# Kernel optimization log

Measured on AMD Instinct MI355X. Metric: run time of the kernel, lower is better.

Reference implementation:

```python
import jax, jax.numpy as jnp
import numpy as np
import math

B, T, C, H = 4, 1024, 1024, 16
D = C // H
EPS = 1e-5


def layer_norm(x, w, b):
    mu = jnp.mean(x, axis=-1, keepdims=True)
    var = jnp.mean(jnp.square(x - mu), axis=-1, keepdims=True)
    return (x - mu) * jax.lax.rsqrt(var + EPS) * w + b


def setup_inputs() -> dict:
    key = jax.random.key(0)
    ks = jax.random.split(key, 8)
    s = 0.02
    return {
        "x": jax.random.normal(ks[0], (B, T, C), jnp.float32),
        "attention_mask": jnp.ones((B, T), jnp.float32),
        "ln1_w": jnp.ones((C,), jnp.float32),
        "ln1_b": jnp.zeros((C,), jnp.float32),
        "w_attn": jax.random.normal(ks[1], (C, 3 * C), jnp.float32) * s,
        "b_attn": jnp.zeros((3 * C,), jnp.float32),
        "w_proj": jax.random.normal(ks[2], (C, C), jnp.float32) * s,
        "b_proj": jnp.zeros((C,), jnp.float32),
        "threshold": jnp.float32(0.0005),  # (layer_idx+1)/n_layer * final_token_threshold
        "ln2_w": jnp.ones((C,), jnp.float32),
        "ln2_b": jnp.zeros((C,), jnp.float32),
        "w_fc": jax.random.normal(ks[3], (C, 4 * C), jnp.float32) * s,
        "b_fc": jnp.zeros((4 * C,), jnp.float32),
        "w_fc2": jax.random.normal(ks[4], (4 * C, C), jnp.float32) * s,
        "b_fc2": jnp.zeros((C,), jnp.float32),
    }


def reference(x, attention_mask, ln1_w, ln1_b, w_attn, b_attn, w_proj, b_proj,
              threshold, ln2_w, ln2_b, w_fc, b_fc, w_fc2, b_fc2):
    # ---- attention (eval mode, dropout=0; hard masking_mode) ----
    h = layer_norm(x, ln1_w, ln1_b)
    qkv = h @ w_attn + b_attn                      # (B,T,3C)
    q, k, v = jnp.split(qkv, 3, axis=-1)
    q = q.reshape(B, T, H, D).transpose(0, 2, 1, 3)  # (B,H,T,D)
    k = k.reshape(B, T, H, D).transpose(0, 2, 1, 3)
    v = v.reshape(B, T, H, D).transpose(0, 2, 1, 3)

    scale = 1.0 / math.sqrt(D)
    logits = jnp.einsum("bhqd,bhkd->bhqk", q, k) * scale  # (B,H,T,T)
    causal = jnp.tril(jnp.ones((T, T), bool))
    neg_inf = jnp.float32(-jnp.inf)
    logits = jnp.where(causal[None, None], logits, neg_inf)
    # key-side validity mask (applied in original's manual pass; mask is all-ones
    # here so flash-path y == softmax(causal logits) @ v as well)
    logits = jnp.where(attention_mask[:, None, None, :] == 0, neg_inf, logits)
    att = jax.nn.softmax(logits, axis=-1)

    y = jnp.einsum("bhqk,bhkd->bhqd", att, v)      # (B,H,T,D)
    importance = att.mean(axis=1).mean(axis=1)     # (B,T): mean over heads, then queries

    y = y.transpose(0, 2, 1, 3).reshape(B, T, C)
    x = x + (y @ w_proj + b_proj)

    # ---- hard pruning mask ----
    pruning_mask = (importance >= threshold).astype(x.dtype)
    combined_mask = attention_mask * pruning_mask
    x = x * combined_mask[:, :, None]

    # ---- MLP ----
    h2 = layer_norm(x, ln2_w, ln2_b)
    f = jax.nn.gelu(h2 @ w_fc + b_fc, approximate=False)
    x = x + (f @ w_fc2 + b_fc2)

    pruning_loss = jnp.float32(0.0)  # hard mode -> always 0
    return (x, combined_mask, pruning_loss)
```

## Files before the change

kernel.cpp:

```cpp
#include <hip/hip_runtime.h>
#include <cstdint>
#include <cstring>

typedef unsigned short u16;
typedef short bf16x8 __attribute__((ext_vector_type(8)));
typedef float f32x4 __attribute__((ext_vector_type(4)));

#define MFMA16(a,b,c) __builtin_amdgcn_mfma_f32_16x16x32_bf16(a,b,c,0,0,0)


__device__ __forceinline__ u16 f2bf(float f) {
  union { float f; uint32_t u; } un; un.f = f;
  uint32_t u = un.u;
  u += 0x7FFFu + ((u >> 16) & 1u);
  return (u16)(u >> 16);
}

__device__ __forceinline__ float bf2f(u16 h) {
  union { uint32_t u; float f; } un; un.u = ((uint32_t)h) << 16;
  return un.f;
}

__device__ __forceinline__ float gelu_fast(float v) {
  float u = 0.7978845608028654f * (v + 0.044715f * v * v * v);
  float e = __expf(2.f * u);
  float th = 1.f - __fdividef(2.f, e + 1.f);
  return 0.5f * v * (1.f + th);
}

__device__ __forceinline__ void gl_lds16(const void* g, void* l) {
  __builtin_amdgcn_global_load_lds(
      (__attribute__((address_space(1))) void*)(const_cast<void*>(g)),
      (__attribute__((address_space(3))) void*)l, 16, 0, 0);
}


__global__ __launch_bounds__(256) void transpose_all(
    const float* __restrict__ wa, const float* __restrict__ wp,
    const float* __restrict__ wf, const float* __restrict__ wf2,
    u16* __restrict__ wat, u16* __restrict__ wpt,
    u16* __restrict__ wft, u16* __restrict__ wf2t)
{
  __shared__ float tile[32][33];
  int id = blockIdx.x;
  const float* W; u16* Wt; int K, N, bx, by;
  if (id < 3072)      { W = wa;  Wt = wat;  K = 1024; N = 3072; bx = id % 96;  by = id / 96; }
  else if (id < 4096) { id -= 3072; W = wp;  Wt = wpt;  K = 1024; N = 1024; bx = id % 32; by = id / 32; }
  else if (id < 8192) { id -= 4096; W = wf;  Wt = wft;  K = 1024; N = 4096; bx = id % 128; by = id / 128; }
  else                { id -= 8192; W = wf2; Wt = wf2t; K = 4096; N = 1024; bx = id % 32; by = id / 32; }
  int kt = by * 32, nt = bx * 32;
  int tx = threadIdx.x, ty = threadIdx.y;
#pragma unroll
  for (int i = 0; i < 4; ++i)
    tile[ty + i * 8][tx] = W[(size_t)(kt + ty + i * 8) * N + nt + tx];
  __syncthreads();
#pragma unroll
  for (int i = 0; i < 4; ++i)
    Wt[(size_t)(nt + ty + i * 8) * K + kt + tx] = f2bf(tile[tx][ty + i * 8]);
}


__global__ __launch_bounds__(256) void ln_bf16(
    const float* __restrict__ x, const float* __restrict__ wt,
    const float* __restrict__ bs, u16* __restrict__ out)
{
  int row = blockIdx.x;
  int tid = threadIdx.x, lane = tid & 63, w = tid >> 6;
  const float* xr = x + (size_t)row * 1024;
  float4 v = *(const float4*)(xr + tid * 4);
  float s = v.x + v.y + v.z + v.w;
  float sq = v.x * v.x + v.y * v.y + v.z * v.z + v.w * v.w;
#pragma unroll
  for (int o = 1; o < 64; o <<= 1) { s += __shfl_xor(s, o); sq += __shfl_xor(sq, o); }
  __shared__ float ls[4], lq[4];
  if (lane == 0) { ls[w] = s; lq[w] = sq; }
  __syncthreads();
  s = ls[0] + ls[1] + ls[2] + ls[3];
  sq = lq[0] + lq[1] + lq[2] + lq[3];
  float mu = s * (1.f / 1024.f);
  float var = sq * (1.f / 1024.f) - mu * mu;
  float rstd = rsqrtf(var + 1e-5f);
  float4 wv = *(const float4*)(wt + tid * 4);
  float4 bv = *(const float4*)(bs + tid * 4);
  ushort4 o4;
  o4.x = f2bf((v.x - mu) * rstd * wv.x + bv.x);
  o4.y = f2bf((v.y - mu) * rstd * wv.y + bv.y);
  o4.z = f2bf((v.z - mu) * rstd * wv.z + bv.z);
  o4.w = f2bf((v.w - mu) * rstd * wv.w + bv.w);
  *(ushort4*)(out + (size_t)row * 1024 + tid * 4) = o4;
}


__device__ __forceinline__ void gemm_mainloop_db(
    const u16* __restrict__ Abase, const u16* __restrict__ Bbase,
    int lda, int ldb, int nIter, f32x4 acc[4][4])
{
  __shared__ __align__(16) u16 lA[2][128 * 32];
  __shared__ __align__(16) u16 lB[2][128 * 32];

  const int tid = threadIdx.x;
  const int lane = tid & 63;
  const int w = tid >> 6;
  const int wr = (w >> 1) * 64;
  const int wc = (w & 1) * 64;
  const int laneM = lane & 15;
  const int laneK = (lane >> 4) * 8;

#pragma unroll
  for (int i = 0; i < 4; ++i)
#pragma unroll
    for (int j = 0; j < 4; ++j)
      acc[i][j] = f32x4{0.f, 0.f, 0.f, 0.f};

  const int off0 = w * 1024 + lane * 16;
  const int off1 = off0 + 4096;
  const int rA0 = off0 >> 6, cb0 = off0 & 63;
  const int rA1 = off1 >> 6, cb1 = off1 & 63;

  const size_t sA = (size_t)lda * 2;
  const size_t sB = (size_t)ldb * 2;
  const char* pA0 = (const char*)Abase + (size_t)rA0 * sA + cb0;
  const char* pA1 = (const char*)Abase + (size_t)rA1 * sA + cb1;
  const char* pB0 = (const char*)Bbase + (size_t)rA0 * sB + cb0;
  const char* pB1 = (const char*)Bbase + (size_t)rA1 * sB + cb1;
  char* dA0 = (char*)&lA[0][0] + off0;
  char* dA1 = (char*)&lA[0][0] + off1;
  char* dB0 = (char*)&lB[0][0] + off0;
  char* dB1 = (char*)&lB[0][0] + off1;

  gl_lds16(pA0, dA0); gl_lds16(pA1, dA1);
  gl_lds16(pB0, dB0); gl_lds16(pB1, dB1);
  pA0 += 64; pA1 += 64; pB0 += 64; pB1 += 64;
  __syncthreads();

  for (int it = 0; it < nIter; ++it) {
    const int cur = it & 1;
    const int nb = cur ^ 1;
    if (it + 1 < nIter) {
      gl_lds16(pA0, dA0 + nb * 8192);
      gl_lds16(pA1, dA1 + nb * 8192);
      gl_lds16(pB0, dB0 + nb * 8192);
      gl_lds16(pB1, dB1 + nb * 8192);
      pA0 += 64; pA1 += 64; pB0 += 64; pB1 += 64;
    }
    const u16* aRd = &lA[cur][(wr + laneM) * 32 + laneK];
    const u16* bRd = &lB[cur][(wc + laneM) * 32 + laneK];
    bf16x8 af[4], bfr[4];
#pragma unroll
    for (int t = 0; t < 4; ++t) {
      af[t]  = *(const bf16x8*)(aRd + t * 16 * 32);
      bfr[t] = *(const bf16x8*)(bRd + t * 16 * 32);
    }
#pragma unroll
    for (int i = 0; i < 4; ++i)
#pragma unroll
      for (int j = 0; j < 4; ++j)
        acc[i][j] = MFMA16(af[i], bfr[j], acc[i][j]);
    if (it + 1 < nIter) __syncthreads();
  }
}


__global__ __launch_bounds__(256, 4) void gemm_qkv(
    const u16* __restrict__ A, const u16* __restrict__ Bt,
    const float* __restrict__ bias,
    u16* __restrict__ qo, u16* __restrict__ ko, u16* __restrict__ vo)
{
  f32x4 acc[4][4];
  int m0 = blockIdx.y * 128, n0 = blockIdx.x * 128;
  gemm_mainloop_db(A + (size_t)m0 * 1024, Bt + (size_t)n0 * 1024, 1024, 1024, 32, acc);
  const int lane = threadIdx.x & 63, w = threadIdx.x >> 6;
  const int wr = (w >> 1) * 64, wc = (w & 1) * 64;
  const int laneM = lane & 15, q4 = lane >> 4;
  const int which = (n0 >> 10);
#pragma unroll
  for (int ti = 0; ti < 4; ++ti) {
#pragma unroll
    for (int tj = 0; tj < 4; ++tj) {
      int n = n0 + wc + tj * 16 + laneM;
      int c = n & 1023;
      int hh = c >> 6, d = c & 63;
      float bval = bias[n];
      if (which == 2) {
        int m0r = m0 + wr + ti * 16 + q4 * 4;
        int b = m0r >> 10, t0 = m0r & 1023;
        ushort4 o4;
        o4.x = f2bf(acc[ti][tj][0] + bval);
        o4.y = f2bf(acc[ti][tj][1] + bval);
        o4.z = f2bf(acc[ti][tj][2] + bval);
        o4.w = f2bf(acc[ti][tj][3] + bval);
        *(ushort4*)&vo[((size_t)((b * 16 + hh) * 64 + d)) * 1024 + t0] = o4;
      } else {
        u16* dst = (which == 0) ? qo : ko;
#pragma unroll
        for (int r = 0; r < 4; ++r) {
          int m = m0 + wr + ti * 16 + q4 * 4 + r;
          int b = m >> 10, t = m & 1023;
          dst[((size_t)((b * 16 + hh) * 1024 + t)) * 64 + d] = f2bf(acc[ti][tj][r] + bval);
        }
      }
    }
  }
}

__global__ __launch_bounds__(256, 4) void gemm_proj(
    const u16* __restrict__ A, const u16* __restrict__ Bt,
    const float* __restrict__ bias, const float* __restrict__ xin,
    const float* __restrict__ maskv, float* __restrict__ x2)
{
  f32x4 acc[4][4];
  int m0 = blockIdx.y * 128, n0 = blockIdx.x * 128;
  gemm_mainloop_db(A + (size_t)m0 * 1024, Bt + (size_t)n0 * 1024, 1024, 1024, 32, acc);
  const int lane = threadIdx.x & 63, w = threadIdx.x >> 6;
  const int wr = (w >> 1) * 64, wc = (w & 1) * 64;
  const int laneM = lane & 15, q4 = lane >> 4;
#pragma unroll
  for (int ti = 0; ti < 4; ++ti) {
#pragma unroll
    for (int tj = 0; tj < 4; ++tj) {
      int n = n0 + wc + tj * 16 + laneM;
      float bval = bias[n];
#pragma unroll
      for (int r = 0; r < 4; ++r) {
        int m = m0 + wr + ti * 16 + q4 * 4 + r;
        float v = xin[(size_t)m * 1024 + n] + acc[ti][tj][r] + bval;
        x2[(size_t)m * 1024 + n] = v * maskv[m];
      }
    }
  }
}

__global__ __launch_bounds__(256, 4) void gemm_fc(
    const u16* __restrict__ A, const u16* __restrict__ Bt,
    const float* __restrict__ bias, u16* __restrict__ fo)
{
  f32x4 acc[4][4];
  int m0 = blockIdx.y * 128, n0 = blockIdx.x * 128;
  gemm_mainloop_db(A + (size_t)m0 * 1024, Bt + (size_t)n0 * 1024, 1024, 1024, 32, acc);
  const int lane = threadIdx.x & 63, w = threadIdx.x >> 6;
  const int wr = (w >> 1) * 64, wc = (w & 1) * 64;
  const int laneM = lane & 15, q4 = lane >> 4;
#pragma unroll
  for (int ti = 0; ti < 4; ++ti) {
#pragma unroll
    for (int tj = 0; tj < 4; ++tj) {
      int n = n0 + wc + tj * 16 + laneM;
      float bval = bias[n];
#pragma unroll
      for (int r = 0; r < 4; ++r) {
        int m = m0 + wr + ti * 16 + q4 * 4 + r;
        fo[(size_t)m * 4096 + n] = f2bf(gelu_fast(acc[ti][tj][r] + bval));
      }
    }
  }
}

__global__ __launch_bounds__(256, 4) void gemm_fc2_splitk(
    const u16* __restrict__ A, const u16* __restrict__ Bt,
    u16* __restrict__ pall)
{
  int id = blockIdx.x;
  int r = id & 7, j = id >> 3;
  int mt = r * 4 + (j >> 5);
  int rem = j & 31;
  int n0 = (rem & 7) * 128;
  int kz = rem >> 3;
  int m0 = mt * 128;
  f32x4 acc[4][4];
  gemm_mainloop_db(A + (size_t)m0 * 4096 + kz * 1024,
                   Bt + (size_t)n0 * 4096 + kz * 1024, 4096, 4096, 32, acc);
  u16* p = pall + (size_t)kz * 4096 * 1024;
  const int lane = threadIdx.x & 63, w = threadIdx.x >> 6;
  const int wr = (w >> 1) * 64, wc = (w & 1) * 64;
  const int laneM = lane & 15, q4 = lane >> 4;
#pragma unroll
  for (int ti = 0; ti < 4; ++ti) {
#pragma unroll
    for (int tj = 0; tj < 4; ++tj) {
      int n = n0 + wc + tj * 16 + laneM;
#pragma unroll
      for (int r2 = 0; r2 < 4; ++r2) {
        int m = m0 + wr + ti * 16 + q4 * 4 + r2;
        p[(size_t)m * 1024 + n] = f2bf(acc[ti][tj][r2]);
      }
    }
  }
}

__global__ __launch_bounds__(256) void fc2_finalize(
    const float* __restrict__ x2, const float* __restrict__ bias,
    const u16* __restrict__ pall, float* __restrict__ out)
{
  int i = blockIdx.x * 256 + threadIdx.x;
  int col4 = i & 255;
  float4 a = ((const float4*)x2)[i];
  float4 b = ((const float4*)bias)[col4];
  float s0 = a.x + b.x, s1 = a.y + b.y, s2 = a.z + b.z, s3 = a.w + b.w;
#pragma unroll
  for (int z = 0; z < 4; ++z) {
    ushort4 u = ((const ushort4*)(pall + (size_t)z * 4194304))[i];
    s0 += bf2f(u.x); s1 += bf2f(u.y); s2 += bf2f(u.z); s3 += bf2f(u.w);
  }
  float4 o; o.x = s0; o.y = s1; o.z = s2; o.w = s3;
  ((float4*)out)[i] = o;
}


__global__ __launch_bounds__(256) void attn_fwd(
    const u16* __restrict__ qb, const u16* __restrict__ kb, const u16* __restrict__ vtb,
    u16* __restrict__ yb, float* __restrict__ part)
{
  const int bh = blockIdx.x;
  const int qbi = 7 - blockIdx.y;
  const int b = bh >> 4, h = bh & 15;
  const int tid = threadIdx.x, lane = tid & 63, w = tid >> 6;
  const int q0 = qbi * 128;
  const int laneM = lane & 15, q4 = lane >> 4;
  const float scale = 0.125f;

  __shared__ __align__(16) u16 lK[64 * 72];
  __shared__ __align__(16) u16 lV[64 * 72];
  __shared__ __align__(16) u16 lP[4][32 * 72];

  bf16x8 qf[2][2];
#pragma unroll
  for (int qs = 0; qs < 2; ++qs) {
    const u16* qrow = qb + ((size_t)(bh * 1024 + q0 + w * 32 + qs * 16 + laneM)) * 64 + q4 * 8;
    qf[qs][0] = *(const bf16x8*)qrow;
    qf[qs][1] = *(const bf16x8*)(qrow + 32);
  }

  const int nkt = 2 * qbi + 2;
  const int srow = tid >> 3;
  const int scol = (tid & 7) * 8;
  const u16* kbase = kb + (size_t)bh * 65536;
  const u16* vbase = vtb + (size_t)bh * 65536;

  float lrow[2][4] = {{0.f,0.f,0.f,0.f},{0.f,0.f,0.f,0.f}};
  for (int kt = 0; kt < nkt; ++kt) {
#pragma unroll
    for (int p = 0; p < 2; ++p) {
      int row = srow + p * 32;
      *(uint4*)&lK[row * 72 + scol] =
          *(const uint4*)(kbase + (size_t)(kt * 64 + row) * 64 + scol);
    }
    __syncthreads();
#pragma unroll
    for (int tj = 0; tj < 4; ++tj) {
      const u16* kp = &lK[(tj * 16 + laneM) * 72 + q4 * 8];
      bf16x8 k0 = *(const bf16x8*)kp;
      bf16x8 k1 = *(const bf16x8*)(kp + 32);
      int kc = kt * 64 + tj * 16 + laneM;
#pragma unroll
      for (int qs = 0; qs < 2; ++qs) {
        f32x4 z = {0.f, 0.f, 0.f, 0.f};
        z = MFMA16(qf[qs][0], k0, z);
        z = MFMA16(qf[qs][1], k1, z);
#pragma unroll
        for (int r = 0; r < 4; ++r) {
          int qg = q0 + w * 32 + qs * 16 + q4 * 4 + r;
          lrow[qs][r] += (kc <= qg) ? __expf(z[r] * scale) : 0.f;
        }
      }
    }
    __syncthreads();
  }
  float linv[2][4];
#pragma unroll
  for (int qs = 0; qs < 2; ++qs)
#pragma unroll
    for (int r = 0; r < 4; ++r) {
      float s = lrow[qs][r];
      s += __shfl_xor(s, 1); s += __shfl_xor(s, 2);
      s += __shfl_xor(s, 4); s += __shfl_xor(s, 8);
      linv[qs][r] = 1.f / s;
    }

  f32x4 o_[2][4];
#pragma unroll
  for (int qs = 0; qs < 2; ++qs)
#pragma unroll
    for (int dt = 0; dt < 4; ++dt) o_[qs][dt] = f32x4{0.f, 0.f, 0.f, 0.f};

  for (int kt = 0; kt < nkt; ++kt) {
#pragma unroll
    for (int p = 0; p < 2; ++p) {
      int row = srow + p * 32;
      *(uint4*)&lK[row * 72 + scol] =
          *(const uint4*)(kbase + (size_t)(kt * 64 + row) * 64 + scol);
      *(uint4*)&lV[row * 72 + scol] =
          *(const uint4*)(vbase + (size_t)row * 1024 + kt * 64 + scol);
    }
    __syncthreads();
    u16* lPw = &lP[w][0];
#pragma unroll
    for (int tj = 0; tj < 4; ++tj) {
      const u16* kp = &lK[(tj * 16 + laneM) * 72 + q4 * 8];
      bf16x8 k0 = *(const bf16x8*)kp;
      bf16x8 k1 = *(const bf16x8*)(kp + 32);
      int kc = kt * 64 + tj * 16 + laneM;
      float cs = 0.f;
#pragma unroll
      for (int qs = 0; qs < 2; ++qs) {
        f32x4 z = {0.f, 0.f, 0.f, 0.f};
        z = MFMA16(qf[qs][0], k0, z);
        z = MFMA16(qf[qs][1], k1, z);
#pragma unroll
        for (int r = 0; r < 4; ++r) {
          int qg = q0 + w * 32 + qs * 16 + q4 * 4 + r;
          float pv = (kc <= qg) ? __expf(z[r] * scale) * linv[qs][r] : 0.f;
          cs += pv;
          lPw[(qs * 16 + q4 * 4 + r) * 72 + tj * 16 + laneM] = f2bf(pv);
        }
      }
      cs += __shfl_xor(cs, 16);
      cs += __shfl_xor(cs, 32);
      if (lane < 16)
        atomicAdd(&part[(size_t)bh * 1024 + kt * 64 + tj * 16 + lane], cs);
    }
#pragma unroll
    for (int ss = 0; ss < 2; ++ss) {
#pragma unroll
      for (int qs = 0; qs < 2; ++qs) {
        bf16x8 pf = *(const bf16x8*)&lP[w][(qs * 16 + laneM) * 72 + ss * 32 + q4 * 8];
#pragma unroll
        for (int dt = 0; dt < 4; ++dt) {
          bf16x8 vf = *(const bf16x8*)&lV[(dt * 16 + laneM) * 72 + ss * 32 + q4 * 8];
          o_[qs][dt] = MFMA16(pf, vf, o_[qs][dt]);
        }
      }
    }
    __syncthreads();
  }

#pragma unroll
  for (int qs = 0; qs < 2; ++qs)
#pragma unroll
    for (int dt = 0; dt < 4; ++dt)
#pragma unroll
      for (int r = 0; r < 4; ++r) {
        int qg = q0 + w * 32 + qs * 16 + q4 * 4 + r;
        yb[((size_t)(b * 1024 + qg)) * 1024 + h * 64 + dt * 16 + laneM] = f2bf(o_[qs][dt][r]);
      }
}


__global__ __launch_bounds__(256) void finalize_mask(
    const float* __restrict__ part, const float* __restrict__ amask,
    const float* __restrict__ thr, float* __restrict__ mask_ws,
    float* __restrict__ out_mask, float* __restrict__ out_loss)
{
  int i = blockIdx.x * 256 + threadIdx.x;
  if (i >= 4096) return;
  int b = i >> 10;
  int t = i & 1023;
  float s = 0.f;
#pragma unroll
  for (int hh = 0; hh < 16; ++hh) s += part[(size_t)(b * 16 + hh) * 1024 + t];
  float imp = s * (1.0f / 16384.0f);
  float mv = (imp >= thr[0]) ? amask[i] : 0.f;
  mask_ws[i] = mv;
  out_mask[i] = mv;
  if (i == 0) out_loss[0] = 0.f;
}


extern "C" void kernel_launch(void* const* d_in, const int* in_sizes, int n_in,
                              void* d_out, int out_size, void* d_ws, size_t ws_size,
                              hipStream_t stream) {
  const float* x      = (const float*)d_in[0];
  const float* amask  = (const float*)d_in[1];
  const float* ln1w   = (const float*)d_in[2];
  const float* ln1b   = (const float*)d_in[3];
  const float* w_attn = (const float*)d_in[4];
  const float* b_attn = (const float*)d_in[5];
  const float* w_proj = (const float*)d_in[6];
  const float* b_proj = (const float*)d_in[7];
  const float* thr    = (const float*)d_in[8];
  const float* ln2w   = (const float*)d_in[9];
  const float* ln2b   = (const float*)d_in[10];
  const float* w_fc   = (const float*)d_in[11];
  const float* b_fc   = (const float*)d_in[12];
  const float* w_fc2  = (const float*)d_in[13];
  const float* b_fc2  = (const float*)d_in[14];
  float* out = (float*)d_out;

  char* ws = (char*)d_ws;
  size_t off = 0;
  auto alloc = [&](size_t bytes) -> char* {
    char* p = ws + off;
    off += (bytes + 255) & ~(size_t)255;
    return p;
  };
  u16* wattnT = (u16*)alloc((size_t)3072 * 1024 * 2);
  u16* wprojT = (u16*)alloc((size_t)1024 * 1024 * 2);
  u16* wfcT   = (u16*)alloc((size_t)4096 * 1024 * 2);
  u16* wfc2T  = (u16*)alloc((size_t)1024 * 4096 * 2);
  u16* hbuf   = (u16*)alloc((size_t)4096 * 1024 * 2);
  u16* qbuf   = (u16*)alloc((size_t)64 * 1024 * 64 * 2);
  u16* kbuf   = (u16*)alloc((size_t)64 * 1024 * 64 * 2);
  u16* vtbuf  = (u16*)alloc((size_t)64 * 64 * 1024 * 2);
  u16* ybuf   = (u16*)alloc((size_t)4096 * 1024 * 2);
  float* part = (float*)alloc((size_t)64 * 1024 * 4);
  float* maskws = (float*)alloc((size_t)4096 * 4);
  float* x2   = (float*)alloc((size_t)4096 * 1024 * 4);
  u16* h2     = (u16*)alloc((size_t)4096 * 1024 * 2);
  u16* fbuf   = (u16*)alloc((size_t)4096 * 4096 * 2);

  u16* pall = qbuf;

  transpose_all<<<12288, dim3(32, 8), 0, stream>>>(
      w_attn, w_proj, w_fc, w_fc2, wattnT, wprojT, wfcT, wfc2T);

  hipMemsetAsync(part, 0, (size_t)64 * 1024 * 4, stream);

  ln_bf16<<<4096, 256, 0, stream>>>(x, ln1w, ln1b, hbuf);

  gemm_qkv<<<dim3(24, 32), 256, 0, stream>>>(hbuf, wattnT, b_attn, qbuf, kbuf, vtbuf);

  attn_fwd<<<dim3(64, 8), 256, 0, stream>>>(qbuf, kbuf, vtbuf, ybuf, part);

  finalize_mask<<<16, 256, 0, stream>>>(part, amask, thr, maskws,
                                        out + 4194304, out + 4198400);

  gemm_proj<<<dim3(8, 32), 256, 0, stream>>>(ybuf, wprojT, b_proj, x, maskws, x2);

  ln_bf16<<<4096, 256, 0, stream>>>(x2, ln2w, ln2b, h2);

  gemm_fc<<<dim3(32, 32), 256, 0, stream>>>(h2, wfcT, b_fc, fbuf);

  gemm_fc2_splitk<<<1024, 256, 0, stream>>>(fbuf, wfc2T, pall);

  fc2_finalize<<<4096, 256, 0, stream>>>(x2, b_fc2, pall, out);
}
```

Before: 353.0 us.

## Restructure attention kernel: 8 waves, double-buffered K/V, LDS column-sum accumulation

The attention kernel now runs 512 threads per block, with each wave owning 16 query rows instead of 32. K and V tiles are double-buffered in LDS, so the next tile's global load is issued before the current tile's MFMA work and stored afterwards. Per-key column sums for the importance score are gathered with shared-memory atomics and flushed to global once per block, replacing many global atomics. A 1D grid with an interleaved query-block mapping pairs long and short causal blocks to balance work across CUs. The cost is more LDS per block and more registers held for the prefetch.

Result: no change. 348.9 us (-1.2%).

```diff
diff --git a/kernel.cpp b/kernel.cpp
--- a/kernel.cpp
+++ b/kernel.cpp
@@ -306,28 +306,34 @@
 }
 
 
-__global__ __launch_bounds__(256) void attn_fwd(
+__global__ __launch_bounds__(512) void attn_fwd(
     const u16* __restrict__ qb, const u16* __restrict__ kb, const u16* __restrict__ vtb,
     u16* __restrict__ yb, float* __restrict__ part)
 {
-  const int bh = blockIdx.x;
-  const int qbi = 7 - blockIdx.y;
+  const int id = blockIdx.x;
+  const int slot = (id & 7) ^ ((id >> 8) & 1);
+  const int qbi = (slot & 1) ? (slot >> 1) : (7 - (slot >> 1));
+  const int bh = id >> 3;
   const int b = bh >> 4, h = bh & 15;
+
   const int tid = threadIdx.x, lane = tid & 63, w = tid >> 6;
   const int q0 = qbi * 128;
   const int laneM = lane & 15, q4 = lane >> 4;
   const float scale = 0.125f;
 
-  __shared__ __align__(16) u16 lK[64 * 72];
-  __shared__ __align__(16) u16 lV[64 * 72];
-  __shared__ __align__(16) u16 lP[4][32 * 72];
-
-  bf16x8 qf[2][2];
-#pragma unroll
-  for (int qs = 0; qs < 2; ++qs) {
-    const u16* qrow = qb + ((size_t)(bh * 1024 + q0 + w * 32 + qs * 16 + laneM)) * 64 + q4 * 8;
-    qf[qs][0] = *(const bf16x8*)qrow;
-    qf[qs][1] = *(const bf16x8*)(qrow + 32);
+  __shared__ __align__(16) u16 lK[2][64 * 72];
+  __shared__ __align__(16) u16 lV[2][64 * 72];
+  __shared__ __align__(16) u16 lP[8][16 * 72];
+  __shared__ float part_s[1024];
+
+  part_s[tid] = 0.f;
+  part_s[tid + 512] = 0.f;
+
+  bf16x8 qf[2];
+  {
+    const u16* qrow = qb + ((size_t)(bh * 1024 + q0 + w * 16 + laneM)) * 64 + q4 * 8;
+    qf[0] = *(const bf16x8*)qrow;
+    qf[1] = *(const bf16x8*)(qrow + 32);
   }
 
   const int nkt = 2 * qbi + 2;
@@ -336,112 +342,109 @@
   const u16* kbase = kb + (size_t)bh * 65536;
   const u16* vbase = vtb + (size_t)bh * 65536;
 
-  float lrow[2][4] = {{0.f,0.f,0.f,0.f},{0.f,0.f,0.f,0.f}};
-  for (int kt = 0; kt < nkt; ++kt) {
-#pragma unroll
-    for (int p = 0; p < 2; ++p) {
-      int row = srow + p * 32;
-      *(uint4*)&lK[row * 72 + scol] =
-          *(const uint4*)(kbase + (size_t)(kt * 64 + row) * 64 + scol);
-    }
+  float lrow[4] = {0.f, 0.f, 0.f, 0.f};
+  {
+    uint4 pk = *(const uint4*)(kbase + (size_t)srow * 64 + scol);
+    *(uint4*)&lK[0][srow * 72 + scol] = pk;
     __syncthreads();
-#pragma unroll
-    for (int tj = 0; tj < 4; ++tj) {
-      const u16* kp = &lK[(tj * 16 + laneM) * 72 + q4 * 8];
-      bf16x8 k0 = *(const bf16x8*)kp;
-      bf16x8 k1 = *(const bf16x8*)(kp + 32);
-      int kc = kt * 64 + tj * 16 + laneM;
-#pragma unroll
-      for (int qs = 0; qs < 2; ++qs) {
+    for (int kt = 0; kt < nkt; ++kt) {
+      const int cur = kt & 1;
+      if (kt + 1 < nkt)
+        pk = *(const uint4*)(kbase + (size_t)((kt + 1) * 64 + srow) * 64 + scol);
+#pragma unroll
+      for (int tj = 0; tj < 4; ++tj) {
+        const u16* kp = &lK[cur][(tj * 16 + laneM) * 72 + q4 * 8];
+        bf16x8 k0 = *(const bf16x8*)kp;
+        bf16x8 k1 = *(const bf16x8*)(kp + 32);
         f32x4 z = {0.f, 0.f, 0.f, 0.f};
-        z = MFMA16(qf[qs][0], k0, z);
-        z = MFMA16(qf[qs][1], k1, z);
+        z = MFMA16(qf[0], k0, z);
+        z = MFMA16(qf[1], k1, z);
+        int kc = kt * 64 + tj * 16 + laneM;
 #pragma unroll
         for (int r = 0; r < 4; ++r) {
-          int qg = q0 + w * 32 + qs * 16 + q4 * 4 + r;
-          lrow[qs][r] += (kc <= qg) ? __expf(z[r] * scale) : 0.f;
+          int qg = q0 + w * 16 + q4 * 4 + r;
+          lrow[r] += (kc <= qg) ? __expf(z[r] * scale) : 0.f;
         }
       }
-    }
+      if (kt + 1 < nkt) *(uint4*)&lK[cur ^ 1][srow * 72 + scol] = pk;
+      __syncthreads();
+    }
+  }
+  float linv[4];
+#pragma unroll
+  for (int r = 0; r < 4; ++r) {
+    float s = lrow[r];
+    s += __shfl_xor(s, 1); s += __shfl_xor(s, 2);
+    s += __shfl_xor(s, 4); s += __shfl_xor(s, 8);
+    linv[r] = 1.f / s;
+  }
+
+  f32x4 o_[4];
+#pragma unroll
+  for (int dt = 0; dt < 4; ++dt) o_[dt] = f32x4{0.f, 0.f, 0.f, 0.f};
+
+  {
+    uint4 pk = *(const uint4*)(kbase + (size_t)srow * 64 + scol);
+    uint4 pv = *(const uint4*)(vbase + (size_t)srow * 1024 + scol);
+    *(uint4*)&lK[0][srow * 72 + scol] = pk;
+    *(uint4*)&lV[0][srow * 72 + scol] = pv;
     __syncthreads();
-  }
-  float linv[2][4];
-#pragma unroll
-  for (int qs = 0; qs < 2; ++qs)
+    for (int kt = 0; kt < nkt; ++kt) {
+      const int cur = kt & 1;
+      if (kt + 1 < nkt) {
+        pk = *(const uint4*)(kbase + (size_t)((kt + 1) * 64 + srow) * 64 + scol);
+        pv = *(const uint4*)(vbase + (size_t)srow * 1024 + (kt + 1) * 64 + scol);
+      }
+      u16* lPw = &lP[w][0];
+#pragma unroll
+      for (int tj = 0; tj < 4; ++tj) {
+        const u16* kp = &lK[cur][(tj * 16 + laneM) * 72 + q4 * 8];
+        bf16x8 k0 = *(const bf16x8*)kp;
+        bf16x8 k1 = *(const bf16x8*)(kp + 32);
+        f32x4 z = {0.f, 0.f, 0.f, 0.f};
+        z = MFMA16(qf[0], k0, z);
+        z = MFMA16(qf[1], k1, z);
+        int kc = kt * 64 + tj * 16 + laneM;
+        float cs = 0.f;
+#pragma unroll
+        for (int r = 0; r < 4; ++r) {
+          int qg = q0 + w * 16 + q4 * 4 + r;
+          float pvf = (kc <= qg) ? __expf(z[r] * scale) * linv[r] : 0.f;
+          cs += pvf;
+          lPw[(q4 * 4 + r) * 72 + tj * 16 + laneM] = f2bf(pvf);
+        }
+        cs += __shfl_xor(cs, 16);
+        cs += __shfl_xor(cs, 32);
+        if (lane < 16) atomicAdd(&part_s[kt * 64 + tj * 16 + lane], cs);
+      }
+#pragma unroll
+      for (int ss = 0; ss < 2; ++ss) {
+        bf16x8 pf = *(const bf16x8*)&lP[w][laneM * 72 + ss * 32 + q4 * 8];
+#pragma unroll
+        for (int dt = 0; dt < 4; ++dt) {
+          bf16x8 vf = *(const bf16x8*)&lV[cur][(dt * 16 + laneM) * 72 + ss * 32 + q4 * 8];
+          o_[dt] = MFMA16(pf, vf, o_[dt]);
+        }
+      }
+      if (kt + 1 < nkt) {
+        *(uint4*)&lK[cur ^ 1][srow * 72 + scol] = pk;
+        *(uint4*)&lV[cur ^ 1][srow * 72 + scol] = pv;
+      }
+      __syncthreads();
+    }
+  }
+
+  const int kmax = nkt * 64;
+  for (int i = tid; i < kmax; i += 512)
+    atomicAdd(&part[(size_t)bh * 1024 + i], part_s[i]);
+
+#pragma unroll
+  for (int dt = 0; dt < 4; ++dt)
 #pragma unroll
     for (int r = 0; r < 4; ++r) {
-      float s = lrow[qs][r];
-      s += __shfl_xor(s, 1); s += __shfl_xor(s, 2);
-      s += __shfl_xor(s, 4); s += __shfl_xor(s, 8);
-      linv[qs][r] = 1.f / s;
-    }
-
-  f32x4 o_[2][4];
-#pragma unroll
-  for (int qs = 0; qs < 2; ++qs)
-#pragma unroll
-    for (int dt = 0; dt < 4; ++dt) o_[qs][dt] = f32x4{0.f, 0.f, 0.f, 0.f};
-
-  for (int kt = 0; kt < nkt; ++kt) {
-#pragma unroll
-    for (int p = 0; p < 2; ++p) {
-      int row = srow + p * 32;
-      *(uint4*)&lK[row * 72 + scol] =
-          *(const uint4*)(kbase + (size_t)(kt * 64 + row) * 64 + scol);
-      *(uint4*)&lV[row * 72 + scol] =
-          *(const uint4*)(vbase + (size_t)row * 1024 + kt * 64 + scol);
-    }
-    __syncthreads();
-    u16* lPw = &lP[w][0];
-#pragma unroll
-    for (int tj = 0; tj < 4; ++tj) {
-      const u16* kp = &lK[(tj * 16 + laneM) * 72 + q4 * 8];
-      bf16x8 k0 = *(const bf16x8*)kp;
-      bf16x8 k1 = *(const bf16x8*)(kp + 32);
-      int kc = kt * 64 + tj * 16 + laneM;
-      float cs = 0.f;
-#pragma unroll
-      for (int qs = 0; qs < 2; ++qs) {
-        f32x4 z = {0.f, 0.f, 0.f, 0.f};
-        z = MFMA16(qf[qs][0], k0, z);
-        z = MFMA16(qf[qs][1], k1, z);
-#pragma unroll
-        for (int r = 0; r < 4; ++r) {
-          int qg = q0 + w * 32 + qs * 16 + q4 * 4 + r;
-          float pv = (kc <= qg) ? __expf(z[r] * scale) * linv[qs][r] : 0.f;
-          cs += pv;
-          lPw[(qs * 16 + q4 * 4 + r) * 72 + tj * 16 + laneM] = f2bf(pv);
-        }
-      }
-      cs += __shfl_xor(cs, 16);
-      cs += __shfl_xor(cs, 32);
-      if (lane < 16)
-        atomicAdd(&part[(size_t)bh * 1024 + kt * 64 + tj * 16 + lane], cs);
-    }
-#pragma unroll
-    for (int ss = 0; ss < 2; ++ss) {
-#pragma unroll
-      for (int qs = 0; qs < 2; ++qs) {
-        bf16x8 pf = *(const bf16x8*)&lP[w][(qs * 16 + laneM) * 72 + ss * 32 + q4 * 8];
-#pragma unroll
-        for (int dt = 0; dt < 4; ++dt) {
-          bf16x8 vf = *(const bf16x8*)&lV[(dt * 16 + laneM) * 72 + ss * 32 + q4 * 8];
-          o_[qs][dt] = MFMA16(pf, vf, o_[qs][dt]);
-        }
-      }
-    }
-    __syncthreads();
-  }
-
-#pragma unroll
-  for (int qs = 0; qs < 2; ++qs)
-#pragma unroll
-    for (int dt = 0; dt < 4; ++dt)
-#pragma unroll
-      for (int r = 0; r < 4; ++r) {
-        int qg = q0 + w * 32 + qs * 16 + q4 * 4 + r;
-        yb[((size_t)(b * 1024 + qg)) * 1024 + h * 64 + dt * 16 + laneM] = f2bf(o_[qs][dt][r]);
-      }
+      int qg = q0 + w * 16 + q4 * 4 + r;
+      yb[((size_t)(b * 1024 + qg)) * 1024 + h * 64 + dt * 16 + laneM] = f2bf(o_[dt][r]);
+    }
 }
 
 
@@ -518,7 +521,7 @@
 
   gemm_qkv<<<dim3(24, 32), 256, 0, stream>>>(hbuf, wattnT, b_attn, qbuf, kbuf, vtbuf);
 
-  attn_fwd<<<dim3(64, 8), 256, 0, stream>>>(qbuf, kbuf, vtbuf, ybuf, part);
+  attn_fwd<<<512, 512, 0, stream>>>(qbuf, kbuf, vtbuf, ybuf, part);
 
   finalize_mask<<<16, 256, 0, stream>>>(part, amask, thr, maskws,
                                         out + 4194304, out + 4198400);
```
